# Kernel tuning notes

Hardware: AMD Instinct MI355X
Metric: run time of the kernel (lower is better)

## Reference

```python
import jax, jax.numpy as jnp
import numpy as np
from functools import partial

STEPLIM = 10
TOL = 1e-4


def _knn1(pc1, pc2):
    """1-NN of each point in pc1 (B,N1,3) against pc2 (B,N2,3).
    Same math as torch: L2 norm of broadcasted diff, topk(k=1, smallest),
    expressed via the |a|^2+|b|^2-2ab expansion to avoid the (B,N1,N2,3) diff."""
    sq1 = jnp.sum(pc1 * pc1, axis=-1)                       # (B,N1)
    sq2 = jnp.sum(pc2 * pc2, axis=-1)                       # (B,N2)
    cross = jnp.einsum('bnd,bmd->bnm', pc1, pc2)            # (B,N1,N2)
    d2 = jnp.maximum(sq1[..., :, None] + sq2[..., None, :] - 2.0 * cross, 0.0)
    idx = jnp.argmin(d2, axis=-1)                           # (B,N1)
    dmin = jnp.sqrt(jnp.take_along_axis(d2, idx[..., None], axis=-1)[..., 0])
    return dmin, idx


def _points_transform(pts1, pts2):
    """Kabsch/SVD rigid fit: R, t such that R @ pts1 + t ~= pts2 (EPnP._points_transform)."""
    c1 = jnp.mean(pts1, axis=-2, keepdims=True)             # (B,1,3)
    c2 = jnp.mean(pts2, axis=-2, keepdims=True)
    q1 = pts1 - c1
    q2 = pts2 - c2
    H = jnp.einsum('bni,bnj->bij', q1, q2)                  # (B,3,3) covariance
    U, S, Vh = jnp.linalg.svd(H)
    V = jnp.swapaxes(Vh, -1, -2)
    d = jnp.sign(jnp.linalg.det(jnp.einsum('bik,bjk->bij', V, U)))  # det(V U^T)
    sgn = jnp.stack([jnp.ones_like(d), jnp.ones_like(d), d], axis=-1)  # fix reflection
    R = jnp.einsum('bik,bk,bjk->bij', V, sgn, U)            # V diag(1,1,d) U^T
    t = c2 - jnp.einsum('bij,bnj->bni', R, c1)              # (B,1,3)
    return R, t


def _apply(R, t, pts):
    return jnp.einsum('bij,bnj->bni', R, pts) + t


def _icp(p1, p2):
    B = p1.shape[0]

    def step(carry, _):
        temppc, err, done = carry
        dmin, idx = _knn1(temppc, p2)
        errnew = jnp.mean(dmin, axis=-1)                    # (B,)
        # torch: first iteration err is None -> no break check; err0=inf makes cond False (nan < tol)
        cond = jnp.all(jnp.abs((errnew - err) / err) < TOL)
        new_done = done | cond
        matched = jax.vmap(lambda pc, i: pc[i])(p2, idx)    # (B,N1,3) gather of p2
        R, t = _points_transform(temppc, matched)
        temppc_new = _apply(R, t, temppc)
        temppc = jnp.where(new_done, temppc, temppc_new)
        err = jnp.where(new_done, err, errnew)
        return (temppc, err, new_done), None

    err0 = jnp.full((B,), jnp.inf, dtype=p1.dtype)
    done0 = jnp.array(False)
    (temppc, _, _), _ = jax.lax.scan(step, (p1, err0, done0), None, length=STEPLIM + 1)
    R, t = _points_transform(p1, temppc)
    return jnp.concatenate([R, jnp.swapaxes(t, -1, -2)], axis=-1)  # (B,3,4) = [R | t]


def setup_inputs() -> dict:
    key = jax.random.key(0)
    k1, k2 = jax.random.split(key)
    p1 = jax.random.normal(k1, (1, 8192, 3), dtype=jnp.float32)
    p2 = jax.random.normal(k2, (1, 8192, 3), dtype=jnp.float32)
    return {"p1": p1, "p2": p2}


def reference(p1, p2):
    return _icp(p1, p2)
```

## Files before the change

kernel.cpp:

```cpp
#include <hip/hip_runtime.h>
#include <float.h>
#include <math.h>

#define N_PTS 8192
#define NB    256
#define NT    512
#define QPB   32
#define QPT   8
#define NRG   128
#define RC    64
#define STEPS 11
#define TOLV  1e-4

#define PADSLOT(i) ((i) + ((i) >> 6))
#define SC_SZ (N_PTS + N_PTS/64)

#define WS_P2F    0
#define WS_TEMPPC 131072
#define WS_BPA    229376
#define WS_BPB    262144
#define WS_ERRH   294912
#define WS_DONEH  295040

__device__ void kabsch3(const double H[3][3], const double c1[3], const double c2[3],
                        double R[3][3], double t[3]) {
    double A[3][3];
    for (int i = 0; i < 3; ++i)
        for (int j = 0; j < 3; ++j) {
            double sacc = 0.0;
            for (int k = 0; k < 3; ++k) sacc += H[k][i] * H[k][j];
            A[i][j] = sacc;
        }
    double V[3][3] = {{1,0,0},{0,1,0},{0,0,1}};
    for (int sweep = 0; sweep < 6; ++sweep) {
        const int PQ[3][2] = {{0,1},{0,2},{1,2}};
        for (int mm = 0; mm < 3; ++mm) {
            int p = PQ[mm][0], q = PQ[mm][1];
            double apq = A[p][q];
            if (fabs(apq) < 1e-300) continue;
            double app = A[p][p], aqq = A[q][q];
            double tau = (aqq - app) / (2.0 * apq);
            double tt = (tau >= 0.0) ? 1.0 / (tau + sqrt(1.0 + tau*tau))
                                     : 1.0 / (tau - sqrt(1.0 + tau*tau));
            double c = 1.0 / sqrt(1.0 + tt*tt), s = tt * c;
            A[p][p] = app - tt * apq;
            A[q][q] = aqq + tt * apq;
            A[p][q] = 0.0; A[q][p] = 0.0;
            int k = 3 - p - q;
            double akp = A[k][p], akq = A[k][q];
            A[k][p] = c*akp - s*akq; A[p][k] = A[k][p];
            A[k][q] = s*akp + c*akq; A[q][k] = A[k][q];
            for (int r = 0; r < 3; ++r) {
                double vp = V[r][p], vq = V[r][q];
                V[r][p] = c*vp - s*vq;
                V[r][q] = s*vp + c*vq;
            }
        }
    }
    double lam[3] = {A[0][0], A[1][1], A[2][2]};
    int ord[3] = {0,1,2};
    for (int i = 0; i < 2; ++i)
        for (int j = i+1; j < 3; ++j)
            if (lam[ord[j]] > lam[ord[i]]) { int tmp = ord[i]; ord[i] = ord[j]; ord[j] = tmp; }
    double v0[3] = {V[0][ord[0]], V[1][ord[0]], V[2][ord[0]]};
    double v1[3] = {V[0][ord[1]], V[1][ord[1]], V[2][ord[1]]};
    double v2[3] = {V[0][ord[2]], V[1][ord[2]], V[2][ord[2]]};

    double u0[3], u1[3], hv2[3];
    for (int i = 0; i < 3; ++i) u0[i] = H[i][0]*v0[0] + H[i][1]*v0[1] + H[i][2]*v0[2];
    double n0 = sqrt(u0[0]*u0[0] + u0[1]*u0[1] + u0[2]*u0[2]);
    n0 = fmax(n0, 1e-300);
    for (int i = 0; i < 3; ++i) u0[i] /= n0;

    for (int i = 0; i < 3; ++i) u1[i] = H[i][0]*v1[0] + H[i][1]*v1[1] + H[i][2]*v1[2];
    double d01 = u1[0]*u0[0] + u1[1]*u0[1] + u1[2]*u0[2];
    for (int i = 0; i < 3; ++i) u1[i] -= d01 * u0[i];
    double n1 = sqrt(u1[0]*u1[0] + u1[1]*u1[1] + u1[2]*u1[2]);
    n1 = fmax(n1, 1e-300);
    for (int i = 0; i < 3; ++i) u1[i] /= n1;

    double u2[3] = {u0[1]*u1[2] - u0[2]*u1[1],
                    u0[2]*u1[0] - u0[0]*u1[2],
                    u0[0]*u1[1] - u0[1]*u1[0]};
    for (int i = 0; i < 3; ++i) hv2[i] = H[i][0]*v2[0] + H[i][1]*v2[1] + H[i][2]*v2[2];
    if (hv2[0]*u2[0] + hv2[1]*u2[1] + hv2[2]*u2[2] < 0.0) {
        v2[0] = -v2[0]; v2[1] = -v2[1]; v2[2] = -v2[2];
    }
    double cx = v1[1]*v2[2] - v1[2]*v2[1];
    double cy = v1[2]*v2[0] - v1[0]*v2[2];
    double cz = v1[0]*v2[1] - v1[1]*v2[0];
    double detV = v0[0]*cx + v0[1]*cy + v0[2]*cz;
    double dsg = (detV < 0.0) ? -1.0 : 1.0;

    for (int i = 0; i < 3; ++i)
        for (int j = 0; j < 3; ++j)
            R[i][j] = v0[i]*u0[j] + v1[i]*u1[j] + dsg * v2[i]*u2[j];
    for (int i = 0; i < 3; ++i)
        t[i] = c2[i] - (R[i][0]*c1[0] + R[i][1]*c1[1] + R[i][2]*c1[2]);
}

__device__ __forceinline__ void build_H(const double s[16], double c1[3], double c2[3],
                                        double H[3][3]) {
    const double Nn = (double)N_PTS;
    c1[0] = s[1]/Nn; c1[1] = s[2]/Nn; c1[2] = s[3]/Nn;
    c2[0] = s[4]/Nn; c2[1] = s[5]/Nn; c2[2] = s[6]/Nn;
    for (int i = 0; i < 3; ++i)
        for (int j = 0; j < 3; ++j)
            H[i][j] = s[7 + 3*i + j] - Nn * c1[i] * c2[j];
}

__global__ __launch_bounds__(NT, 2) void icp_step(
    const float* __restrict__ p1, const float* __restrict__ p2,
    float4* __restrict__ p2f, float* __restrict__ temppc,
    const double* __restrict__ bp_prev, double* __restrict__ bp_cur,
    double* __restrict__ err_hist, int* __restrict__ done_hist, int it)
{
    __shared__ float4 sCand[SC_SZ];
    __shared__ float4 sQ[QPB];
    __shared__ float  sWB[8][QPT];
    __shared__ int    sWI[8][QPT];
    __shared__ float  sRt[12];
    __shared__ int    sDone;
    const int tid = threadIdx.x, bid = blockIdx.x;

    const int latched = (it > 0) ? done_hist[it-1] : 0;
    const bool scan_possible = (it < STEPS) && !latched;

    if (scan_possible) {
        if (it == 0) {
            #pragma unroll
            for (int k = 0; k < 16; ++k) {
                int i = tid + NT*k;
                float x = p2[3*i], y = p2[3*i+1], z = p2[3*i+2];
                sCand[PADSLOT(i)] = make_float4(x, y, z, x*x + y*y + z*z);
            }
        } else {
            #pragma unroll
            for (int k = 0; k < 16; ++k) {
                int i = tid + NT*k;
                sCand[PADSLOT(i)] = p2f[i];
            }
        }
    }

    int done = 0;
    if (it == 0) {
        __syncthreads();
        if (bid == 0 && tid == 0) { err_hist[0] = __builtin_inf(); done_hist[0] = 0; }
        if (tid < QPB) {
            int i = bid*QPB + tid;
            p2f[i] = sCand[PADSLOT(i)];
        }
    } else if (latched) {
        done = 1;
        if (bid == 0 && tid == 0) { done_hist[it] = 1; err_hist[it] = err_hist[it-1]; }
    } else {
        if (tid < 64) {
            double sv[16];
            #pragma unroll
            for (int k = 0; k < 16; ++k) sv[k] = 0.0;
            #pragma unroll
            for (int jj = 0; jj < 4; ++jj) {
                const double* row = bp_prev + (tid + 64*jj)*16;
                #pragma unroll
                for (int k = 0; k < 16; ++k) sv[k] += row[k];
            }
            #pragma unroll
            for (int off = 1; off < 64; off <<= 1) {
                #pragma unroll
                for (int k = 0; k < 16; ++k) sv[k] += __shfl_xor(sv[k], off, 64);
            }
            if (tid == 0) {
                double errnew = sv[0] / (double)N_PTS;
                double err = err_hist[it-1];
                double rel = fabs((errnew - err) / err);
                int nd = (rel < TOLV) ? 1 : 0;
                if (bid == 0) { done_hist[it] = nd; err_hist[it] = nd ? err : errnew; }
                sDone = nd;
                if (!nd) {
                    double c1[3], c2[3], H[3][3], Rm[3][3], tv[3];
                    build_H(sv, c1, c2, H);
                    kabsch3(H, c1, c2, Rm, tv);
                    for (int i = 0; i < 3; ++i) {
                        sRt[3*i]   = (float)Rm[i][0];
                        sRt[3*i+1] = (float)Rm[i][1];
                        sRt[3*i+2] = (float)Rm[i][2];
                        sRt[9+i]   = (float)tv[i];
                    }
                }
            }
        }
        __syncthreads();
        done = sDone;
    }

    if (done && it < STEPS) return;

    if (tid < QPB) {
        int q = bid*QPB + tid;
        float x, y, z;
        if (it == 0) {
            x = p1[3*q]; y = p1[3*q+1]; z = p1[3*q+2];
            temppc[3*q] = x; temppc[3*q+1] = y; temppc[3*q+2] = z;
        } else {
            x = temppc[3*q]; y = temppc[3*q+1]; z = temppc[3*q+2];
            if (!done) {
                float nx = fmaf(sRt[0], x, fmaf(sRt[1], y, fmaf(sRt[2], z, sRt[9])));
                float ny = fmaf(sRt[3], x, fmaf(sRt[4], y, fmaf(sRt[5], z, sRt[10])));
                float nz = fmaf(sRt[6], x, fmaf(sRt[7], y, fmaf(sRt[8], z, sRt[11])));
                x = nx; y = ny; z = nz;
                temppc[3*q] = x; temppc[3*q+1] = y; temppc[3*q+2] = z;
            }
        }
        sQ[tid] = make_float4(x, y, z, x*x + y*y + z*z);
    }
    __syncthreads();

    if (it == STEPS) {
        if (tid < 64) {
            double vals[16];
            if (tid < 32) {
                int q = bid*QPB + tid;
                float ax = p1[3*q], ay = p1[3*q+1], az = p1[3*q+2];
                float4 b4 = sQ[tid];
                vals[0] = 0.0;
                vals[1] = (double)ax;   vals[2] = (double)ay;   vals[3] = (double)az;
                vals[4] = (double)b4.x; vals[5] = (double)b4.y; vals[6] = (double)b4.z;
                vals[7]  = (double)ax*b4.x; vals[8]  = (double)ax*b4.y; vals[9]  = (double)ax*b4.z;
                vals[10] = (double)ay*b4.x; vals[11] = (double)ay*b4.y; vals[12] = (double)ay*b4.z;
                vals[13] = (double)az*b4.x; vals[14] = (double)az*b4.y; vals[15] = (double)az*b4.z;
            } else {
                #pragma unroll
                for (int k = 0; k < 16; ++k) vals[k] = 0.0;
            }
            #pragma unroll
            for (int off = 1; off < 32; off <<= 1) {
                #pragma unroll
                for (int k = 0; k < 16; ++k) vals[k] += __shfl_xor(vals[k], off, 64);
            }
            if (tid == 0) {
                double* d = bp_cur + bid*16;
                #pragma unroll
                for (int k = 0; k < 16; ++k) d[k] = vals[k];
            }
        }
        return;
    }

    const int g = tid >> 7;
    const int r = tid & 127;
    float qx[QPT], qy[QPT], qz[QPT];
    #pragma unroll
    for (int k = 0; k < QPT; ++k) {
        float4 a = sQ[QPT*g + k];
        qx[k] = -2.f*a.x; qy[k] = -2.f*a.y; qz[k] = -2.f*a.z;
    }
    float best[QPT]; int bi[QPT];
    #pragma unroll
    for (int k = 0; k < QPT; ++k) { best[k] = FLT_MAX; bi[k] = 0; }

    const int sb = 65*r;
    const int gb = 64*r;

#define PROC8(SJ, JJ)                                                 \
    {                                                                 \
        _Pragma("unroll")                                             \
        for (int k = 0; k < QPT; ++k) {                               \
            float v = fmaf(qx[k], (SJ).x, (SJ).w);                    \
            v = fmaf(qy[k], (SJ).y, v);                               \
            v = fmaf(qz[k], (SJ).z, v);                               \
            if (v < best[k]) { best[k] = v; bi[k] = (JJ); }           \
        }                                                             \
    }

    float4 cur = sCand[sb];
    #pragma unroll 4
    for (int j = 0; j < RC - 1; ++j) {
        float4 nxt = sCand[sb + j + 1];
        PROC8(cur, gb + j);
        cur = nxt;
    }
    PROC8(cur, gb + RC - 1);
#undef PROC8

    #pragma unroll
    for (int off = 1; off < 64; off <<= 1) {
        #pragma unroll
        for (int k = 0; k < QPT; ++k) {
            float ov = __shfl_xor(best[k], off, 64);
            int   oi = __shfl_xor(bi[k],  off, 64);
            if (ov < best[k] || (ov == best[k] && oi < bi[k])) { best[k] = ov; bi[k] = oi; }
        }
    }
    const int w = tid >> 6;
    if ((tid & 63) == 0) {
        #pragma unroll
        for (int k = 0; k < QPT; ++k) { sWB[w][k] = best[k]; sWI[w][k] = bi[k]; }
    }
    __syncthreads();

    if (tid < 64) {
        double vals[16];
        if (tid < 32) {
            int q = tid;
            int gg = q >> 3, k = q & 7;
            float bv = sWB[2*gg][k];   int bix = sWI[2*gg][k];
            float ov = sWB[2*gg+1][k]; int oi  = sWI[2*gg+1][k];
            if (ov < bv || (ov == bv && oi < bix)) { bv = ov; bix = oi; }
            float4 a4 = sQ[q];
            float d2 = fmaxf(bv + a4.w, 0.0f);
            float dmin = sqrtf(d2);
            float4 b4 = p2f[bix];
            vals[0] = (double)dmin;
            vals[1] = (double)a4.x; vals[2] = (double)a4.y; vals[3] = (double)a4.z;
            vals[4] = (double)b4.x; vals[5] = (double)b4.y; vals[6] = (double)b4.z;
            vals[7]  = (double)a4.x*b4.x; vals[8]  = (double)a4.x*b4.y; vals[9]  = (double)a4.x*b4.z;
            vals[10] = (double)a4.y*b4.x; vals[11] = (double)a4.y*b4.y; vals[12] = (double)a4.y*b4.z;
            vals[13] = (double)a4.z*b4.x; vals[14] = (double)a4.z*b4.y; vals[15] = (double)a4.z*b4.z;
        } else {
            #pragma unroll
            for (int k = 0; k < 16; ++k) vals[k] = 0.0;
        }
        #pragma unroll
        for (int off = 1; off < 32; off <<= 1) {
            #pragma unroll
            for (int k = 0; k < 16; ++k) vals[k] += __shfl_xor(vals[k], off, 64);
        }
        if (tid == 0) {
            double* d = bp_cur + bid*16;
            #pragma unroll
            for (int k = 0; k < 16; ++k) d[k] = vals[k];
        }
    }
}

__global__ void icp_final(const double* __restrict__ bp, float* __restrict__ out) {
    int tid = threadIdx.x;
    double sv[16];
    #pragma unroll
    for (int k = 0; k < 16; ++k) sv[k] = 0.0;
    #pragma unroll
    for (int j = 0; j < 4; ++j) {
        const double* row = bp + (tid + 64*j)*16;
        #pragma unroll
        for (int k = 0; k < 16; ++k) sv[k] += row[k];
    }
    #pragma unroll
    for (int off = 1; off < 64; off <<= 1) {
        #pragma unroll
        for (int k = 0; k < 16; ++k) sv[k] += __shfl_xor(sv[k], off, 64);
    }
    if (tid == 0) {
        double c1[3], c2[3], H[3][3], Rm[3][3], tv[3];
        build_H(sv, c1, c2, H);
        kabsch3(H, c1, c2, Rm, tv);
        for (int i = 0; i < 3; ++i) {
            out[4*i + 0] = (float)Rm[i][0];
            out[4*i + 1] = (float)Rm[i][1];
            out[4*i + 2] = (float)Rm[i][2];
            out[4*i + 3] = (float)tv[i];
        }
    }
}

extern "C" void kernel_launch(void* const* d_in, const int* in_sizes, int n_in,
                              void* d_out, int out_size, void* d_ws, size_t ws_size,
                              hipStream_t stream) {
    const float* p1 = (const float*)d_in[0];
    const float* p2 = (const float*)d_in[1];
    float* out = (float*)d_out;
    char* ws = (char*)d_ws;

    float4* p2f       = (float4*)(ws + WS_P2F);
    float*  temppc    = (float*) (ws + WS_TEMPPC);
    double* bpA       = (double*)(ws + WS_BPA);
    double* bpB       = (double*)(ws + WS_BPB);
    double* err_hist  = (double*)(ws + WS_ERRH);
    int*    done_hist = (int*)   (ws + WS_DONEH);

    for (int it = 0; it <= STEPS; ++it) {
        double* cur  = (it & 1) ? bpB : bpA;
        double* prev = (it & 1) ? bpA : bpB;
        icp_step<<<NB, NT, 0, stream>>>(p1, p2, p2f, temppc, prev, cur,
                                        err_hist, done_hist, it);
    }
    icp_final<<<1, 64, 0, stream>>>(bpB, out);
}
```

Baseline: 305.5 us.

## Reduce with a last-block ticket and fixed-point atomics, and scan minimums without indices

New measurement: 748.8 us. +145.1%, slower.

```diff
diff --git a/kernel.cpp b/kernel.cpp
--- a/kernel.cpp
+++ b/kernel.cpp
@@ -7,7 +7,6 @@
 #define NT    512
 #define QPB   32
 #define QPT   8
-#define NRG   128
 #define RC    64
 #define STEPS 11
 #define TOLV  1e-4
@@ -15,82 +14,85 @@
 #define PADSLOT(i) ((i) + ((i) >> 6))
 #define SC_SZ (N_PTS + N_PTS/64)
 
+#define FXSCALE   68719476736.0
+#define INVFX     (1.0 / 68719476736.0)
+
 #define WS_P2F    0
 #define WS_TEMPPC 131072
-#define WS_BPA    229376
-#define WS_BPB    262144
-#define WS_ERRH   294912
-#define WS_DONEH  295040
-
-__device__ void kabsch3(const double H[3][3], const double c1[3], const double c2[3],
-                        double R[3][3], double t[3]) {
-    double A[3][3];
+#define WS_ACC    229376
+#define WS_GS     229760
+
+struct GS { float Rt[12]; double err; int done; int pad; };
+
+__device__ void kabsch3f(const float H[3][3], const float c1[3], const float c2[3],
+                         float R[3][3], float t[3]) {
+    float A[3][3];
     for (int i = 0; i < 3; ++i)
         for (int j = 0; j < 3; ++j) {
-            double sacc = 0.0;
+            float sacc = 0.0f;
             for (int k = 0; k < 3; ++k) sacc += H[k][i] * H[k][j];
             A[i][j] = sacc;
         }
-    double V[3][3] = {{1,0,0},{0,1,0},{0,0,1}};
+    float V[3][3] = {{1,0,0},{0,1,0},{0,0,1}};
     for (int sweep = 0; sweep < 6; ++sweep) {
         const int PQ[3][2] = {{0,1},{0,2},{1,2}};
         for (int mm = 0; mm < 3; ++mm) {
             int p = PQ[mm][0], q = PQ[mm][1];
-            double apq = A[p][q];
-            if (fabs(apq) < 1e-300) continue;
-            double app = A[p][p], aqq = A[q][q];
-            double tau = (aqq - app) / (2.0 * apq);
-            double tt = (tau >= 0.0) ? 1.0 / (tau + sqrt(1.0 + tau*tau))
-                                     : 1.0 / (tau - sqrt(1.0 + tau*tau));
-            double c = 1.0 / sqrt(1.0 + tt*tt), s = tt * c;
+            float apq = A[p][q];
+            if (fabsf(apq) < 1e-30f) continue;
+            float app = A[p][p], aqq = A[q][q];
+            float tau = (aqq - app) / (2.0f * apq);
+            float tt = (tau >= 0.0f) ? 1.0f / (tau + sqrtf(1.0f + tau*tau))
+                                     : 1.0f / (tau - sqrtf(1.0f + tau*tau));
+            float c = 1.0f / sqrtf(1.0f + tt*tt), s = tt * c;
             A[p][p] = app - tt * apq;
             A[q][q] = aqq + tt * apq;
-            A[p][q] = 0.0; A[q][p] = 0.0;
+            A[p][q] = 0.0f; A[q][p] = 0.0f;
             int k = 3 - p - q;
-            double akp = A[k][p], akq = A[k][q];
+            float akp = A[k][p], akq = A[k][q];
             A[k][p] = c*akp - s*akq; A[p][k] = A[k][p];
             A[k][q] = s*akp + c*akq; A[q][k] = A[k][q];
             for (int r = 0; r < 3; ++r) {
-                double vp = V[r][p], vq = V[r][q];
+                float vp = V[r][p], vq = V[r][q];
                 V[r][p] = c*vp - s*vq;
                 V[r][q] = s*vp + c*vq;
             }
         }
     }
-    double lam[3] = {A[0][0], A[1][1], A[2][2]};
+    float lam[3] = {A[0][0], A[1][1], A[2][2]};
     int ord[3] = {0,1,2};
     for (int i = 0; i < 2; ++i)
         for (int j = i+1; j < 3; ++j)
             if (lam[ord[j]] > lam[ord[i]]) { int tmp = ord[i]; ord[i] = ord[j]; ord[j] = tmp; }
-    double v0[3] = {V[0][ord[0]], V[1][ord[0]], V[2][ord[0]]};
-    double v1[3] = {V[0][ord[1]], V[1][ord[1]], V[2][ord[1]]};
-    double v2[3] = {V[0][ord[2]], V[1][ord[2]], V[2][ord[2]]};
-
-    double u0[3], u1[3], hv2[3];
+    float v0[3] = {V[0][ord[0]], V[1][ord[0]], V[2][ord[0]]};
+    float v1[3] = {V[0][ord[1]], V[1][ord[1]], V[2][ord[1]]};
+    float v2[3] = {V[0][ord[2]], V[1][ord[2]], V[2][ord[2]]};
+
+    float u0[3], u1[3], hv2[3];
     for (int i = 0; i < 3; ++i) u0[i] = H[i][0]*v0[0] + H[i][1]*v0[1] + H[i][2]*v0[2];
-    double n0 = sqrt(u0[0]*u0[0] + u0[1]*u0[1] + u0[2]*u0[2]);
-    n0 = fmax(n0, 1e-300);
+    float n0 = sqrtf(u0[0]*u0[0] + u0[1]*u0[1] + u0[2]*u0[2]);
+    n0 = fmaxf(n0, 1e-30f);
     for (int i = 0; i < 3; ++i) u0[i] /= n0;
 
     for (int i = 0; i < 3; ++i) u1[i] = H[i][0]*v1[0] + H[i][1]*v1[1] + H[i][2]*v1[2];
-    double d01 = u1[0]*u0[0] + u1[1]*u0[1] + u1[2]*u0[2];
+    float d01 = u1[0]*u0[0] + u1[1]*u0[1] + u1[2]*u0[2];
     for (int i = 0; i < 3; ++i) u1[i] -= d01 * u0[i];
-    double n1 = sqrt(u1[0]*u1[0] + u1[1]*u1[1] + u1[2]*u1[2]);
-    n1 = fmax(n1, 1e-300);
+    float n1 = sqrtf(u1[0]*u1[0] + u1[1]*u1[1] + u1[2]*u1[2]);
+    n1 = fmaxf(n1, 1e-30f);
     for (int i = 0; i < 3; ++i) u1[i] /= n1;
 
-    double u2[3] = {u0[1]*u1[2] - u0[2]*u1[1],
-                    u0[2]*u1[0] - u0[0]*u1[2],
-                    u0[0]*u1[1] - u0[1]*u1[0]};
+    float u2[3] = {u0[1]*u1[2] - u0[2]*u1[1],
+                   u0[2]*u1[0] - u0[0]*u1[2],
+                   u0[0]*u1[1] - u0[1]*u1[0]};
     for (int i = 0; i < 3; ++i) hv2[i] = H[i][0]*v2[0] + H[i][1]*v2[1] + H[i][2]*v2[2];
-    if (hv2[0]*u2[0] + hv2[1]*u2[1] + hv2[2]*u2[2] < 0.0) {
+    if (hv2[0]*u2[0] + hv2[1]*u2[1] + hv2[2]*u2[2] < 0.0f) {
         v2[0] = -v2[0]; v2[1] = -v2[1]; v2[2] = -v2[2];
     }
-    double cx = v1[1]*v2[2] - v1[2]*v2[1];
-    double cy = v1[2]*v2[0] - v1[0]*v2[2];
-    double cz = v1[0]*v2[1] - v1[1]*v2[0];
-    double detV = v0[0]*cx + v0[1]*cy + v0[2]*cz;
-    double dsg = (detV < 0.0) ? -1.0 : 1.0;
+    float cx = v1[1]*v2[2] - v1[2]*v2[1];
+    float cy = v1[2]*v2[0] - v1[0]*v2[2];
+    float cz = v1[0]*v2[1] - v1[1]*v2[0];
+    float detV = v0[0]*cx + v0[1]*cy + v0[2]*cz;
+    float dsg = (detV < 0.0f) ? -1.0f : 1.0f;
 
     for (int i = 0; i < 3; ++i)
         for (int j = 0; j < 3; ++j)
@@ -99,34 +101,42 @@
         t[i] = c2[i] - (R[i][0]*c1[0] + R[i][1]*c1[1] + R[i][2]*c1[2]);
 }
 
-__device__ __forceinline__ void build_H(const double s[16], double c1[3], double c2[3],
-                                        double H[3][3]) {
+__device__ __forceinline__ void build_Hf(const double s[16], float c1[3], float c2[3],
+                                         float H[3][3]) {
     const double Nn = (double)N_PTS;
-    c1[0] = s[1]/Nn; c1[1] = s[2]/Nn; c1[2] = s[3]/Nn;
-    c2[0] = s[4]/Nn; c2[1] = s[5]/Nn; c2[2] = s[6]/Nn;
+    double c1d[3] = {s[1]/Nn, s[2]/Nn, s[3]/Nn};
+    double c2d[3] = {s[4]/Nn, s[5]/Nn, s[6]/Nn};
+    for (int i = 0; i < 3; ++i) { c1[i] = (float)c1d[i]; c2[i] = (float)c2d[i]; }
     for (int i = 0; i < 3; ++i)
         for (int j = 0; j < 3; ++j)
-            H[i][j] = s[7 + 3*i + j] - Nn * c1[i] * c2[j];
+            H[i][j] = (float)(s[7 + 3*i + j] - Nn * c1d[i] * c2d[j]);
+}
+
+__device__ __forceinline__ float dist_val(float4 s, float mx, float my, float mz) {
+    float v = fmaf(mx, s.x, s.w);
+    v = fmaf(my, s.y, v);
+    v = fmaf(mz, s.z, v);
+    return v;
 }
 
 __global__ __launch_bounds__(NT, 2) void icp_step(
     const float* __restrict__ p1, const float* __restrict__ p2,
     float4* __restrict__ p2f, float* __restrict__ temppc,
-    const double* __restrict__ bp_prev, double* __restrict__ bp_cur,
-    double* __restrict__ err_hist, int* __restrict__ done_hist, int it)
+    GS* __restrict__ gs, unsigned long long* __restrict__ acc,
+    unsigned int* __restrict__ ticket, float* __restrict__ out, int it)
 {
     __shared__ float4 sCand[SC_SZ];
     __shared__ float4 sQ[QPB];
-    __shared__ float  sWB[8][QPT];
-    __shared__ int    sWI[8][QPT];
+    __shared__ float  sWmin[8][QPT];
+    __shared__ int    sWin[QPB];
     __shared__ float  sRt[12];
-    __shared__ int    sDone;
     const int tid = threadIdx.x, bid = blockIdx.x;
 
-    const int latched = (it > 0) ? done_hist[it-1] : 0;
-    const bool scan_possible = (it < STEPS) && !latched;
-
-    if (scan_possible) {
+    const int done_prev = (it > 0) ? gs->done : 0;
+    const bool scanning = (it < STEPS);
+    if (scanning && done_prev) return;
+
+    if (scanning) {
         if (it == 0) {
             #pragma unroll
             for (int k = 0; k < 16; ++k) {
@@ -142,59 +152,14 @@
             }
         }
     }
-
-    int done = 0;
-    if (it == 0) {
-        __syncthreads();
-        if (bid == 0 && tid == 0) { err_hist[0] = __builtin_inf(); done_hist[0] = 0; }
-        if (tid < QPB) {
-            int i = bid*QPB + tid;
-            p2f[i] = sCand[PADSLOT(i)];
-        }
-    } else if (latched) {
-        done = 1;
-        if (bid == 0 && tid == 0) { done_hist[it] = 1; err_hist[it] = err_hist[it-1]; }
-    } else {
-        if (tid < 64) {
-            double sv[16];
-            #pragma unroll
-            for (int k = 0; k < 16; ++k) sv[k] = 0.0;
-            #pragma unroll
-            for (int jj = 0; jj < 4; ++jj) {
-                const double* row = bp_prev + (tid + 64*jj)*16;
-                #pragma unroll
-                for (int k = 0; k < 16; ++k) sv[k] += row[k];
-            }
-            #pragma unroll
-            for (int off = 1; off < 64; off <<= 1) {
-                #pragma unroll
-                for (int k = 0; k < 16; ++k) sv[k] += __shfl_xor(sv[k], off, 64);
-            }
-            if (tid == 0) {
-                double errnew = sv[0] / (double)N_PTS;
-                double err = err_hist[it-1];
-                double rel = fabs((errnew - err) / err);
-                int nd = (rel < TOLV) ? 1 : 0;
-                if (bid == 0) { done_hist[it] = nd; err_hist[it] = nd ? err : errnew; }
-                sDone = nd;
-                if (!nd) {
-                    double c1[3], c2[3], H[3][3], Rm[3][3], tv[3];
-                    build_H(sv, c1, c2, H);
-                    kabsch3(H, c1, c2, Rm, tv);
-                    for (int i = 0; i < 3; ++i) {
-                        sRt[3*i]   = (float)Rm[i][0];
-                        sRt[3*i+1] = (float)Rm[i][1];
-                        sRt[3*i+2] = (float)Rm[i][2];
-                        sRt[9+i]   = (float)tv[i];
-                    }
-                }
-            }
-        }
-        __syncthreads();
-        done = sDone;
-    }
-
-    if (done && it < STEPS) return;
+    if (it > 0 && !done_prev && tid < 12) sRt[tid] = gs->Rt[tid];
+    if (tid < QPB) sWin[tid] = 0x7fffffff;
+    __syncthreads();
+
+    if (it == 0 && tid < QPB) {
+        int i = bid*QPB + tid;
+        p2f[i] = sCand[PADSLOT(i)];
+    }
 
     if (tid < QPB) {
         int q = bid*QPB + tid;
@@ -204,7 +169,7 @@
             temppc[3*q] = x; temppc[3*q+1] = y; temppc[3*q+2] = z;
         } else {
             x = temppc[3*q]; y = temppc[3*q+1]; z = temppc[3*q+2];
-            if (!done) {
+            if (!done_prev) {
                 float nx = fmaf(sRt[0], x, fmaf(sRt[1], y, fmaf(sRt[2], z, sRt[9])));
                 float ny = fmaf(sRt[3], x, fmaf(sRt[4], y, fmaf(sRt[5], z, sRt[10])));
                 float nz = fmaf(sRt[6], x, fmaf(sRt[7], y, fmaf(sRt[8], z, sRt[11])));
@@ -216,9 +181,89 @@
     }
     __syncthreads();
 
-    if (it == STEPS) {
+    double vals[16];
+
+    if (scanning) {
+        const int g = tid >> 7;
+        const int r = tid & 127;
+        float qx[QPT], qy[QPT], qz[QPT];
+        #pragma unroll
+        for (int k = 0; k < QPT; ++k) {
+            float4 a = sQ[QPT*g + k];
+            qx[k] = -2.f*a.x; qy[k] = -2.f*a.y; qz[k] = -2.f*a.z;
+        }
+        float tmin[QPT];
+        #pragma unroll
+        for (int k = 0; k < QPT; ++k) tmin[k] = FLT_MAX;
+
+        const int sb = 65*r;
+        float4 cur = sCand[sb];
+        #pragma unroll 4
+        for (int j = 0; j < RC - 1; ++j) {
+            float4 nxt = sCand[sb + j + 1];
+            #pragma unroll
+            for (int k = 0; k < QPT; ++k)
+                tmin[k] = fminf(tmin[k], dist_val(cur, qx[k], qy[k], qz[k]));
+            cur = nxt;
+        }
+        #pragma unroll
+        for (int k = 0; k < QPT; ++k)
+            tmin[k] = fminf(tmin[k], dist_val(cur, qx[k], qy[k], qz[k]));
+
+        float omin[QPT];
+        #pragma unroll
+        for (int k = 0; k < QPT; ++k) omin[k] = tmin[k];
+
+        #pragma unroll
+        for (int off = 1; off < 64; off <<= 1) {
+            #pragma unroll
+            for (int k = 0; k < QPT; ++k)
+                tmin[k] = fminf(tmin[k], __shfl_xor(tmin[k], off, 64));
+        }
+        const int w = tid >> 6;
+        if ((tid & 63) == 0) {
+            #pragma unroll
+            for (int k = 0; k < QPT; ++k) sWmin[w][k] = tmin[k];
+        }
+        __syncthreads();
+
+        #pragma unroll
+        for (int k = 0; k < QPT; ++k) {
+            float gm = fminf(sWmin[2*g][k], sWmin[2*g+1][k]);
+            if (omin[k] == gm) atomicMin(&sWin[QPT*g + k], r);
+        }
+        __syncthreads();
+
         if (tid < 64) {
-            double vals[16];
+            if (tid < 32) {
+                int q = tid, g2 = q >> 3, k2 = q & 7;
+                float gm = fminf(sWmin[2*g2][k2], sWmin[2*g2+1][k2]);
+                int rw = sWin[q];
+                float4 a4 = sQ[q];
+                float mx = -2.f*a4.x, my = -2.f*a4.y, mz = -2.f*a4.z;
+                int bix = -1;
+                const int sbw = 65*rw;
+                #pragma unroll 8
+                for (int j = 0; j < RC; ++j) {
+                    float v = dist_val(sCand[sbw + j], mx, my, mz);
+                    if (v == gm && bix < 0) bix = RC*rw + j;
+                }
+                float d2 = fmaxf(gm + a4.w, 0.0f);
+                float dmin = sqrtf(d2);
+                float4 b4 = sCand[PADSLOT(bix)];
+                vals[0] = (double)dmin;
+                vals[1] = (double)a4.x; vals[2] = (double)a4.y; vals[3] = (double)a4.z;
+                vals[4] = (double)b4.x; vals[5] = (double)b4.y; vals[6] = (double)b4.z;
+                vals[7]  = (double)a4.x*b4.x; vals[8]  = (double)a4.x*b4.y; vals[9]  = (double)a4.x*b4.z;
+                vals[10] = (double)a4.y*b4.x; vals[11] = (double)a4.y*b4.y; vals[12] = (double)a4.y*b4.z;
+                vals[13] = (double)a4.z*b4.x; vals[14] = (double)a4.z*b4.y; vals[15] = (double)a4.z*b4.z;
+            } else {
+                #pragma unroll
+                for (int k = 0; k < 16; ++k) vals[k] = 0.0;
+            }
+        }
+    } else {
+        if (tid < 64) {
             if (tid < 32) {
                 int q = bid*QPB + tid;
                 float ax = p1[3*q], ay = p1[3*q+1], az = p1[3*q+2];
@@ -233,132 +278,64 @@
                 #pragma unroll
                 for (int k = 0; k < 16; ++k) vals[k] = 0.0;
             }
-            #pragma unroll
-            for (int off = 1; off < 32; off <<= 1) {
+        }
+    }
+
+    if (tid < 64) {
+        #pragma unroll
+        for (int off = 1; off < 32; off <<= 1) {
+            #pragma unroll
+            for (int k = 0; k < 16; ++k) vals[k] += __shfl_xor(vals[k], off, 64);
+        }
+        if (tid == 0) {
+            #pragma unroll
+            for (int k = 0; k < 16; ++k) {
+                long long fx = __double2ll_rn(vals[k] * FXSCALE);
+                atomicAdd(&acc[k], (unsigned long long)fx);
+            }
+            __threadfence();
+            unsigned int old = atomicAdd(ticket, 1u);
+            if (old == NB - 1) {
+                double sv[16];
                 #pragma unroll
-                for (int k = 0; k < 16; ++k) vals[k] += __shfl_xor(vals[k], off, 64);
-            }
-            if (tid == 0) {
-                double* d = bp_cur + bid*16;
-                #pragma unroll
-                for (int k = 0; k < 16; ++k) d[k] = vals[k];
-            }
-        }
-        return;
-    }
-
-    const int g = tid >> 7;
-    const int r = tid & 127;
-    float qx[QPT], qy[QPT], qz[QPT];
-    #pragma unroll
-    for (int k = 0; k < QPT; ++k) {
-        float4 a = sQ[QPT*g + k];
-        qx[k] = -2.f*a.x; qy[k] = -2.f*a.y; qz[k] = -2.f*a.z;
-    }
-    float best[QPT]; int bi[QPT];
-    #pragma unroll
-    for (int k = 0; k < QPT; ++k) { best[k] = FLT_MAX; bi[k] = 0; }
-
-    const int sb = 65*r;
-    const int gb = 64*r;
-
-#define PROC8(SJ, JJ)                                                 \
-    {                                                                 \
-        _Pragma("unroll")                                             \
-        for (int k = 0; k < QPT; ++k) {                               \
-            float v = fmaf(qx[k], (SJ).x, (SJ).w);                    \
-            v = fmaf(qy[k], (SJ).y, v);                               \
-            v = fmaf(qz[k], (SJ).z, v);                               \
-            if (v < best[k]) { best[k] = v; bi[k] = (JJ); }           \
-        }                                                             \
-    }
-
-    float4 cur = sCand[sb];
-    #pragma unroll 4
-    for (int j = 0; j < RC - 1; ++j) {
-        float4 nxt = sCand[sb + j + 1];
-        PROC8(cur, gb + j);
-        cur = nxt;
-    }
-    PROC8(cur, gb + RC - 1);
-#undef PROC8
-
-    #pragma unroll
-    for (int off = 1; off < 64; off <<= 1) {
-        #pragma unroll
-        for (int k = 0; k < QPT; ++k) {
-            float ov = __shfl_xor(best[k], off, 64);
-            int   oi = __shfl_xor(bi[k],  off, 64);
-            if (ov < best[k] || (ov == best[k] && oi < bi[k])) { best[k] = ov; bi[k] = oi; }
-        }
-    }
-    const int w = tid >> 6;
-    if ((tid & 63) == 0) {
-        #pragma unroll
-        for (int k = 0; k < QPT; ++k) { sWB[w][k] = best[k]; sWI[w][k] = bi[k]; }
-    }
-    __syncthreads();
-
-    if (tid < 64) {
-        double vals[16];
-        if (tid < 32) {
-            int q = tid;
-            int gg = q >> 3, k = q & 7;
-            float bv = sWB[2*gg][k];   int bix = sWI[2*gg][k];
-            float ov = sWB[2*gg+1][k]; int oi  = sWI[2*gg+1][k];
-            if (ov < bv || (ov == bv && oi < bix)) { bv = ov; bix = oi; }
-            float4 a4 = sQ[q];
-            float d2 = fmaxf(bv + a4.w, 0.0f);
-            float dmin = sqrtf(d2);
-            float4 b4 = p2f[bix];
-            vals[0] = (double)dmin;
-            vals[1] = (double)a4.x; vals[2] = (double)a4.y; vals[3] = (double)a4.z;
-            vals[4] = (double)b4.x; vals[5] = (double)b4.y; vals[6] = (double)b4.z;
-            vals[7]  = (double)a4.x*b4.x; vals[8]  = (double)a4.x*b4.y; vals[9]  = (double)a4.x*b4.z;
-            vals[10] = (double)a4.y*b4.x; vals[11] = (double)a4.y*b4.y; vals[12] = (double)a4.y*b4.z;
-            vals[13] = (double)a4.z*b4.x; vals[14] = (double)a4.z*b4.y; vals[15] = (double)a4.z*b4.z;
-        } else {
-            #pragma unroll
-            for (int k = 0; k < 16; ++k) vals[k] = 0.0;
-        }
-        #pragma unroll
-        for (int off = 1; off < 32; off <<= 1) {
-            #pragma unroll
-            for (int k = 0; k < 16; ++k) vals[k] += __shfl_xor(vals[k], off, 64);
-        }
-        if (tid == 0) {
-            double* d = bp_cur + bid*16;
-            #pragma unroll
-            for (int k = 0; k < 16; ++k) d[k] = vals[k];
-        }
-    }
-}
-
-__global__ void icp_final(const double* __restrict__ bp, float* __restrict__ out) {
-    int tid = threadIdx.x;
-    double sv[16];
-    #pragma unroll
-    for (int k = 0; k < 16; ++k) sv[k] = 0.0;
-    #pragma unroll
-    for (int j = 0; j < 4; ++j) {
-        const double* row = bp + (tid + 64*j)*16;
-        #pragma unroll
-        for (int k = 0; k < 16; ++k) sv[k] += row[k];
-    }
-    #pragma unroll
-    for (int off = 1; off < 64; off <<= 1) {
-        #pragma unroll
-        for (int k = 0; k < 16; ++k) sv[k] += __shfl_xor(sv[k], off, 64);
-    }
-    if (tid == 0) {
-        double c1[3], c2[3], H[3][3], Rm[3][3], tv[3];
-        build_H(sv, c1, c2, H);
-        kabsch3(H, c1, c2, Rm, tv);
-        for (int i = 0; i < 3; ++i) {
-            out[4*i + 0] = (float)Rm[i][0];
-            out[4*i + 1] = (float)Rm[i][1];
-            out[4*i + 2] = (float)Rm[i][2];
-            out[4*i + 3] = (float)tv[i];
+                for (int k = 0; k < 16; ++k) {
+                    unsigned long long u = atomicAdd(&acc[k], 0ULL);
+                    sv[k] = (double)(long long)u * INVFX;
+                    atomicExch(&acc[k], 0ULL);
+                }
+                atomicExch(ticket, 0u);
+                if (scanning) {
+                    double errnew = sv[0] / (double)N_PTS;
+                    double err = (it == 0) ? __builtin_inf() : gs->err;
+                    double rel = fabs((errnew - err) / err);
+                    int nd = (rel < TOLV) ? 1 : 0;
+                    gs->done = nd;
+                    gs->err  = nd ? err : errnew;
+                    if (!nd) {
+                        float c1[3], c2[3], H[3][3], Rm[3][3], tv[3];
+                        build_Hf(sv, c1, c2, H);
+                        kabsch3f(H, c1, c2, Rm, tv);
+                        #pragma unroll
+                        for (int i = 0; i < 3; ++i) {
+                            gs->Rt[3*i]   = Rm[i][0];
+                            gs->Rt[3*i+1] = Rm[i][1];
+                            gs->Rt[3*i+2] = Rm[i][2];
+                            gs->Rt[9+i]   = tv[i];
+                        }
+                    }
+                } else {
+                    float c1[3], c2[3], H[3][3], Rm[3][3], tv[3];
+                    build_Hf(sv, c1, c2, H);
+                    kabsch3f(H, c1, c2, Rm, tv);
+                    #pragma unroll
+                    for (int i = 0; i < 3; ++i) {
+                        out[4*i + 0] = Rm[i][0];
+                        out[4*i + 1] = Rm[i][1];
+                        out[4*i + 2] = Rm[i][2];
+                        out[4*i + 3] = tv[i];
+                    }
+                }
+            }
         }
     }
 }
@@ -371,18 +348,14 @@
     float* out = (float*)d_out;
     char* ws = (char*)d_ws;
 
-    float4* p2f       = (float4*)(ws + WS_P2F);
-    float*  temppc    = (float*) (ws + WS_TEMPPC);
-    double* bpA       = (double*)(ws + WS_BPA);
-    double* bpB       = (double*)(ws + WS_BPB);
-    double* err_hist  = (double*)(ws + WS_ERRH);
-    int*    done_hist = (int*)   (ws + WS_DONEH);
-
+    float4*             p2f    = (float4*)(ws + WS_P2F);
+    float*              temppc = (float*) (ws + WS_TEMPPC);
+    unsigned long long* acc    = (unsigned long long*)(ws + WS_ACC);
+    unsigned int*       ticket = (unsigned int*)(ws + WS_ACC + 16*8);
+    GS*                 gs     = (GS*)    (ws + WS_GS);
+
+    hipMemsetAsync(ws + WS_ACC, 0, 17*8, stream);
     for (int it = 0; it <= STEPS; ++it) {
-        double* cur  = (it & 1) ? bpB : bpA;
-        double* prev = (it & 1) ? bpA : bpB;
-        icp_step<<<NB, NT, 0, stream>>>(p1, p2, p2f, temppc, prev, cur,
-                                        err_hist, done_hist, it);
-    }
-    icp_final<<<1, 64, 0, stream>>>(bpB, out);
-}
+        icp_step<<<NB, NT, 0, stream>>>(p1, p2, p2f, temppc, gs, acc, ticket, out, it);
+    }
+}
```
